# Performance work log

Measured on AMD Instinct MI355X. Metric: run time of the kernel, lower is better.

The kernel has to match this reference:

```python
import jax, jax.numpy as jnp
import numpy as np
import math

# Fixed video latent grid (grid_sizes) and module dims
F_, H_, W_ = 8, 16, 30
FRAME = H_ * W_          # tokens per frame = 480
L = F_ * FRAME           # seq_len = 3840
DIM, NH, HD = 1536, 12, 128
EPS = 1e-6


def _rope_table(maxlen, d):
    # rope_params: angle[t, j] = t / theta^(2j/d), j = 0..d/2-1
    inv = 1.0 / (10000.0 ** (np.arange(0, d, 2, dtype=np.float64) / d))
    return (np.arange(maxlen, dtype=np.float64)[:, None] * inv[None, :]).astype(np.float32)


def _angles(freqs_f, freqs_h, freqs_w):
    # concat per-axis angles -> [F,H,W,HD//2] -> [L, HD//2]
    a = jnp.concatenate([
        jnp.broadcast_to(freqs_f[:F_, None, None, :], (F_, H_, W_, freqs_f.shape[1])),
        jnp.broadcast_to(freqs_h[None, :H_, None, :], (F_, H_, W_, freqs_h.shape[1])),
        jnp.broadcast_to(freqs_w[None, None, :W_, :], (F_, H_, W_, freqs_w.shape[1])),
    ], axis=-1)
    return a.reshape(L, HD // 2)


def _rope(x, ang):
    # x: [B, L, NH, HD]; complex pairs are consecutive along head_dim
    xr, xi = x[..., 0::2], x[..., 1::2]
    c = jnp.cos(ang)[None, :, None, :]
    s = jnp.sin(ang)[None, :, None, :]
    yr = xr * c - xi * s
    yi = xr * s + xi * c
    return jnp.stack([yr, yi], axis=-1).reshape(x.shape)


def _rmsnorm(x, g):
    return x * jax.lax.rsqrt(jnp.mean(x * x, axis=-1, keepdims=True) + EPS) * g


def setup_inputs() -> dict:
    key = jax.random.key(0)
    ks = jax.random.split(key, 6)
    sc = 0.02
    inp = {
        'x': jax.random.normal(ks[0], (1, L, DIM), jnp.float32),
        'Wq': jax.random.normal(ks[1], (DIM, DIM), jnp.float32) * sc,
        'bq': jnp.zeros((DIM,), jnp.float32),
        'Wk': jax.random.normal(ks[2], (DIM, DIM), jnp.float32) * sc,
        'bk': jnp.zeros((DIM,), jnp.float32),
        'Wv': jax.random.normal(ks[3], (DIM, DIM), jnp.float32) * sc,
        'bv': jnp.zeros((DIM,), jnp.float32),
        'Wo': jax.random.normal(ks[4], (DIM, DIM), jnp.float32) * sc,
        'bo': jnp.zeros((DIM,), jnp.float32),
        'gq': jnp.ones((DIM,), jnp.float32),
        'gk': jnp.ones((DIM,), jnp.float32),
        'freqs_f': jnp.asarray(_rope_table(1024, 44)[:F_]),  # 22 complex dims
        'freqs_h': jnp.asarray(_rope_table(1024, 42)[:H_]),  # 21 complex dims
        'freqs_w': jnp.asarray(_rope_table(1024, 42)[:W_]),  # 21 complex dims
    }
    return inp


def reference(x, Wq, bq, Wk, bk, Wv, bv, Wo, bo, gq, gk, freqs_f, freqs_h, freqs_w):
    B = x.shape[0]
    q = _rmsnorm(x @ Wq + bq, gq).reshape(B, L, NH, HD)
    k = _rmsnorm(x @ Wk + bk, gk).reshape(B, L, NH, HD)
    v = (x @ Wv + bv).reshape(B, L, NH, HD)
    ang = _angles(freqs_f, freqs_h, freqs_w)
    q = _rope(q, ang)
    k = _rope(k, ang)
    # frame-level block-causal mask: query frame >= key frame
    frame = jnp.arange(L) // FRAME
    mask = frame[:, None] >= frame[None, :]
    scores = jnp.einsum('bqhd,bkhd->bhqk', q, k) * (1.0 / math.sqrt(HD))
    scores = jnp.where(mask[None, None], scores, -jnp.inf)
    attn = jax.nn.softmax(scores, axis=-1)
    out = jnp.einsum('bhqk,bkhd->bqhd', attn, v).reshape(B, L, DIM)
    return out @ Wo + bo
```

## Files before the change

kernel.cpp:

```cpp
#include <hip/hip_runtime.h>
#include <hip/hip_bf16.h>
#include <math.h>

#define F_    8
#define H_    16
#define W_    30
#define FRAME (H_*W_)
#define L_    (F_*FRAME)
#define DIM   1536
#define NH    12
#define HD    128
#define EPS   1e-6f

#define GM 128
#define GN 128
#define GKT 32

typedef __attribute__((ext_vector_type(8))) short short8;
typedef __attribute__((ext_vector_type(4))) float floatx4;

__device__ __forceinline__ float bf2f(unsigned short u) {
    unsigned int x = ((unsigned int)u) << 16;
    return __uint_as_float(x);
}

__device__ __forceinline__ short f2bs(float f) {
    union { __hip_bfloat16 b; short s; } u;
    u.b = __float2bfloat16(f);
    return u.s;
}

__device__ __forceinline__ bool is_f32_flag(const unsigned int* gq32) {
    return gq32[0] == 0x3F800000u;
}

__device__ __forceinline__ float ldany(const void* p, long i, bool f32) {
    return f32 ? ((const float*)p)[i] : bf2f(((const unsigned short*)p)[i]);
}

__device__ __forceinline__ void gl_lds16(const void* g, void* l) {
    __builtin_amdgcn_global_load_lds(
        (const __attribute__((address_space(1))) unsigned int*)g,
        (__attribute__((address_space(3))) unsigned int*)l,
        16, 0, 0);
}

__global__ __launch_bounds__(256) void k_cossin(const void* Ff, const void* Fh, const void* Fw,
                                                const unsigned int* gq32,
                                                float* cosb, float* sinb) {
    int idx = blockIdx.x * 256 + threadIdx.x;
    if (idx >= L_ * 64) return;
    bool f32 = is_f32_flag(gq32);
    int l = idx >> 6, j = idx & 63;
    int f = l / FRAME;
    int rem = l - f * FRAME;
    int h = rem / W_;
    int w = rem - h * W_;
    float a;
    if (j < 22)      a = ldany(Ff, (long)f * 22 + j, f32);
    else if (j < 43) a = ldany(Fh, (long)h * 21 + (j - 22), f32);
    else             a = ldany(Fw, (long)w * 21 + (j - 43), f32);
    cosb[idx] = cosf(a);
    sinb[idx] = sinf(a);
}

__global__ __launch_bounds__(256) void k_tobf(const void* in, short* out, int n,
                                              const unsigned int* gq32) {
    bool f32 = is_f32_flag(gq32);
    int i = blockIdx.x * 256 + threadIdx.x;
    if (i < n) out[i] = f2bs(ldany(in, i, f32));
}

__global__ __launch_bounds__(256) void k_wt4(const void* W0, const void* W1,
                                             const void* W2, const void* W3,
                                             short* T0, short* T1, short* T2, short* T3,
                                             const unsigned int* gq32) {
    bool f32 = is_f32_flag(gq32);
    int z = blockIdx.z;
    const void* W = z == 0 ? W0 : z == 1 ? W1 : z == 2 ? W2 : W3;
    short* WT     = z == 0 ? T0 : z == 1 ? T1 : z == 2 ? T2 : T3;
    __shared__ float tile[32][33];
    int n0 = blockIdx.x * 32, k0 = blockIdx.y * 32;
    int tx = threadIdx.x & 31, ty = threadIdx.x >> 5;
    for (int i = ty; i < 32; i += 8)
        tile[i][tx] = ldany(W, (long)(k0 + i) * DIM + n0 + tx, f32);
    __syncthreads();
    for (int i = ty; i < 32; i += 8)
        WT[(size_t)(n0 + i) * DIM + k0 + tx] = f2bs(tile[tx][i]);
}

__global__ __launch_bounds__(256) void k_gemm_qkv(const short* A,
                                                  const short* BTq, const short* BTk, const short* BTv,
                                                  const void* bq, const void* bk, const void* bv,
                                                  float* Cq, float* Ck, short* Cv,
                                                  const unsigned int* gq32) {
    bool f32 = is_f32_flag(gq32);
    __shared__ short As[GM * GKT];
    __shared__ short Bs[GN * GKT];

    int sec = blockIdx.x / (DIM / GN);
    int bn  = (blockIdx.x % (DIM / GN)) * GN;
    int bm  = blockIdx.y * GM;
    const short* BT  = sec == 0 ? BTq : sec == 1 ? BTk : BTv;
    const void* bias = sec == 0 ? bq  : sec == 1 ? bk  : bv;

    int tid  = threadIdx.x;
    int wave = tid >> 6, lane = tid & 63;
    int q15 = lane & 15, quad = lane >> 4;
    int wr = wave >> 1, wc = wave & 1;
    int lr = lane >> 2;
    int kc = (lane & 3) * 8;

    floatx4 acc[4][4];
    #pragma unroll
    for (int i = 0; i < 4; ++i)
        #pragma unroll
        for (int j = 0; j < 4; ++j) acc[i][j] = (floatx4)0.f;

    const short* Abase = A  + (size_t)(bm + wave * 32 + lr) * DIM + kc;
    const short* Bbase = BT + (size_t)(bn + wave * 32 + lr) * DIM + kc;
    short* AsW = &As[(wave * 32) * GKT];
    short* BsW = &Bs[(wave * 32) * GKT];

    for (int k0 = 0; k0 < DIM; k0 += GKT) {
        __syncthreads();
        gl_lds16(Abase + k0,                      AsW);
        gl_lds16(Abase + k0 + (size_t)16 * DIM,   AsW + 16 * GKT);
        gl_lds16(Bbase + k0,                      BsW);
        gl_lds16(Bbase + k0 + (size_t)16 * DIM,   BsW + 16 * GKT);
        __syncthreads();

        short8 af[4], bfr[4];
        #pragma unroll
        for (int t = 0; t < 4; ++t) {
            af[t]  = *(const short8*)&As[(wr * 64 + t * 16 + q15) * GKT + quad * 8];
            bfr[t] = *(const short8*)&Bs[(wc * 64 + t * 16 + q15) * GKT + quad * 8];
        }
        #pragma unroll
        for (int i = 0; i < 4; ++i)
            #pragma unroll
            for (int j = 0; j < 4; ++j)
                acc[i][j] = __builtin_amdgcn_mfma_f32_16x16x32_bf16(af[i], bfr[j], acc[i][j], 0, 0, 0);
    }

    #pragma unroll
    for (int i = 0; i < 4; ++i) {
        int row = bm + wr * 64 + i * 16 + quad * 4;
        #pragma unroll
        for (int j = 0; j < 4; ++j) {
            int col = bn + wc * 64 + j * 16 + q15;
            float bv2 = ldany(bias, col, f32);
            #pragma unroll
            for (int r = 0; r < 4; ++r) {
                float v = acc[i][j][r] + bv2;
                size_t oi = (size_t)(row + r) * DIM + col;
                if (sec == 0)      Cq[oi] = v;
                else if (sec == 1) Ck[oi] = v;
                else               Cv[oi] = f2bs(v);
            }
        }
    }
}

__global__ __launch_bounds__(256) void k_gemm_out(const short* A, const short* BT,
                                                  const void* bias, void* Cout,
                                                  const unsigned int* gq32) {
    bool f32 = is_f32_flag(gq32);
    __shared__ short As[GM * GKT];
    __shared__ short Bs[GN * GKT];

    int tid  = threadIdx.x;
    int wave = tid >> 6, lane = tid & 63;
    int q15 = lane & 15, quad = lane >> 4;
    int wr = wave >> 1, wc = wave & 1;
    int lr = lane >> 2;
    int kc = (lane & 3) * 8;

    int bm = blockIdx.y * GM;
    int bn = blockIdx.x * GN;

    floatx4 acc[4][4];
    #pragma unroll
    for (int i = 0; i < 4; ++i)
        #pragma unroll
        for (int j = 0; j < 4; ++j) acc[i][j] = (floatx4)0.f;

    const short* Abase = A  + (size_t)(bm + wave * 32 + lr) * DIM + kc;
    const short* Bbase = BT + (size_t)(bn + wave * 32 + lr) * DIM + kc;
    short* AsW = &As[(wave * 32) * GKT];
    short* BsW = &Bs[(wave * 32) * GKT];

    for (int k0 = 0; k0 < DIM; k0 += GKT) {
        __syncthreads();
        gl_lds16(Abase + k0,                      AsW);
        gl_lds16(Abase + k0 + (size_t)16 * DIM,   AsW + 16 * GKT);
        gl_lds16(Bbase + k0,                      BsW);
        gl_lds16(Bbase + k0 + (size_t)16 * DIM,   BsW + 16 * GKT);
        __syncthreads();

        short8 af[4], bfr[4];
        #pragma unroll
        for (int t = 0; t < 4; ++t) {
            af[t]  = *(const short8*)&As[(wr * 64 + t * 16 + q15) * GKT + quad * 8];
            bfr[t] = *(const short8*)&Bs[(wc * 64 + t * 16 + q15) * GKT + quad * 8];
        }
        #pragma unroll
        for (int i = 0; i < 4; ++i)
            #pragma unroll
            for (int j = 0; j < 4; ++j)
                acc[i][j] = __builtin_amdgcn_mfma_f32_16x16x32_bf16(af[i], bfr[j], acc[i][j], 0, 0, 0);
    }

    #pragma unroll
    for (int i = 0; i < 4; ++i) {
        int row = bm + wr * 64 + i * 16 + quad * 4;
        #pragma unroll
        for (int j = 0; j < 4; ++j) {
            int col = bn + wc * 64 + j * 16 + q15;
            float bv = ldany(bias, col, f32);
            #pragma unroll
            for (int r = 0; r < 4; ++r) {
                float v = acc[i][j][r] + bv;
                size_t oi = (size_t)(row + r) * DIM + col;
                if (f32) ((float*)Cout)[oi] = v;
                else     ((__hip_bfloat16*)Cout)[oi] = __float2bfloat16(v);
            }
        }
    }
}

__global__ __launch_bounds__(256) void k_norm_rope2(const float* qin, const float* kin,
                                                    __hip_bfloat16* qout, __hip_bfloat16* kout,
                                                    const void* gq, const void* gk,
                                                    const float* cosb, const float* sinb,
                                                    const unsigned int* gq32) {
    bool f32 = is_f32_flag(gq32);
    int which = blockIdx.y;
    const float* in = which ? kin : qin;
    __hip_bfloat16* outb = which ? kout : qout;
    const void* g = which ? gk : gq;
    float qk_scale = which ? 1.0f : 0.08838834764831845f;

    int l = blockIdx.x;
    int t = threadIdx.x;
    const float* row = in + (long)l * DIM;
    __hip_bfloat16* orow = outb + (long)l * DIM;

    float ss = 0.f;
    for (int i = t; i < DIM; i += 256) { float xv = row[i]; ss += xv * xv; }
    #pragma unroll
    for (int off = 32; off; off >>= 1) ss += __shfl_xor(ss, off);

    __shared__ float red[4];
    int wid = t >> 6;
    if ((t & 63) == 0) red[wid] = ss;
    __syncthreads();
    float scale = rsqrtf((red[0] + red[1] + red[2] + red[3]) / (float)DIM + EPS) * qk_scale;

    for (int p = t; p < DIM / 2; p += 256) {
        int j = p & 63;
        float c = cosb[l * 64 + j];
        float s = sinb[l * 64 + j];
        float xr = row[2 * p]     * scale * ldany(g, 2 * p,     f32);
        float xi = row[2 * p + 1] * scale * ldany(g, 2 * p + 1, f32);
        orow[2 * p]     = __float2bfloat16(xr * c - xi * s);
        orow[2 * p + 1] = __float2bfloat16(xr * s + xi * c);
    }
}

__global__ __launch_bounds__(256) void k_vt(const short* vbf, short* vtb) {
    __shared__ short tile[32][33];
    int d0 = blockIdx.x * 32;
    int l0 = blockIdx.y * 32;
    int tx = threadIdx.x & 31, ty = threadIdx.x >> 5;
    for (int i = ty; i < 32; i += 8)
        tile[i][tx] = vbf[(size_t)(l0 + i) * DIM + d0 + tx];
    __syncthreads();
    int slot = ((tx & 15) >> 2) * 8 + ((tx >> 4) & 1) * 4 + (tx & 3);
    for (int i = ty; i < 32; i += 8) {
        int d = d0 + i;
        int h = d >> 7, hd = d & 127;
        vtb[((size_t)h * HD + hd) * L_ + l0 + slot] = tile[tx][i];
    }
}

__global__ __launch_bounds__(192, 3) void k_attn7(const short* qbf, const short* kbf,
                                                  const short* vtb,
                                                  float* opart, float* lpart) {
    __shared__ short Ks[2][4][32][32];
    __shared__ short Vs[2][128][32];

    int tid = threadIdx.x;
    int wave = tid >> 6, lane = tid & 63;
    int q15 = lane & 15, quad = lane >> 4;

    int head = blockIdx.x % NH;
    int t = blockIdx.x / NH;
    int rg, kf0, kf1;
    if (t < 30)      { if (t < 25) { rg = 15 + t;        kf0 = 0; kf1 = 3; }
                       else        { rg = 35 + (t - 25); kf0 = 4; kf1 = 7; } }
    else if (t < 40) { int i = t - 30;
                       if (i < 5)  { rg = 10 + i;        kf0 = 0; kf1 = 2; }
                       else        { rg = 30 + (i - 5);  kf0 = 4; kf1 = 6; } }
    else if (t < 50) { int i = t - 40;
                       if (i < 5)  { rg = 5 + i;         kf0 = 0; kf1 = 1; }
                       else        { rg = 25 + (i - 5);  kf0 = 4; kf1 = 5; } }
    else             { int i = t - 50;
                       if (i < 5)  { rg = i;             kf0 = 0; kf1 = 0; }
                       else        { rg = 20 + (i - 5);  kf0 = 4; kf1 = 4; } }

    int qbase  = rg * 96 + wave * 32;
    int kstart = kf0 * FRAME;
    int iters  = (kf1 - kf0 + 1) * (FRAME / 32);
    int slot   = (kf0 == 4) ? 1 : 0;

    const short* kpH = kbf + head * HD;
    const short* vpH = vtb + (size_t)head * HD * L_;

    int sub = lane >> 2;
    int ch  = (lane & 3) * 8;

    for (int i = wave; i < 16; i += 3) {
        if (i < 8) {
            int ks = i >> 1, key = (i & 1) * 16 + sub;
            gl_lds16(kpH + (size_t)(kstart + key) * DIM + ks * 32 + ch,
                     (short*)Ks[0] + i * 512);
        } else {
            int jj = i - 8, d = jj * 16 + sub;
            gl_lds16(vpH + (size_t)d * L_ + kstart + ch,
                     (short*)Vs[0] + jj * 512);
        }
    }

    short8 qf[2][4];
    #pragma unroll
    for (int mi = 0; mi < 2; ++mi)
        #pragma unroll
        for (int ks = 0; ks < 4; ++ks)
            qf[mi][ks] = *(const short8*)(qbf + (size_t)(qbase + mi * 16 + q15) * DIM
                                          + head * HD + ks * 32 + quad * 8);

    floatx4 o[2][8];
    #pragma unroll
    for (int mi = 0; mi < 2; ++mi)
        #pragma unroll
        for (int ct = 0; ct < 8; ++ct) o[mi][ct] = (floatx4)0.f;
    float lp[2] = {0.f, 0.f};

    for (int it = 0; it < iters; ++it) {
        __syncthreads();
        int buf = it & 1;
        if (it + 1 < iters) {
            int kb = kstart + (it + 1) * 32;
            for (int i = wave; i < 16; i += 3) {
                if (i < 8) {
                    int ks = i >> 1, key = (i & 1) * 16 + sub;
                    gl_lds16(kpH + (size_t)(kb + key) * DIM + ks * 32 + ch,
                             (short*)Ks[buf ^ 1] + i * 512);
                } else {
                    int jj = i - 8, d = jj * 16 + sub;
                    gl_lds16(vpH + (size_t)d * L_ + kb + ch,
                             (short*)Vs[buf ^ 1] + jj * 512);
                }
            }
        }

        floatx4 st[2][2];
        #pragma unroll
        for (int nt = 0; nt < 2; ++nt)
            #pragma unroll
            for (int mi = 0; mi < 2; ++mi) st[nt][mi] = (floatx4)0.f;
        #pragma unroll
        for (int ks = 0; ks < 4; ++ks) {
            short8 k0 = *(const short8*)&Ks[buf][ks][q15][quad * 8];
            short8 k1 = *(const short8*)&Ks[buf][ks][16 + q15][quad * 8];
            st[0][0] = __builtin_amdgcn_mfma_f32_16x16x32_bf16(k0, qf[0][ks], st[0][0], 0, 0, 0);
            st[0][1] = __builtin_amdgcn_mfma_f32_16x16x32_bf16(k0, qf[1][ks], st[0][1], 0, 0, 0);
            st[1][0] = __builtin_amdgcn_mfma_f32_16x16x32_bf16(k1, qf[0][ks], st[1][0], 0, 0, 0);
            st[1][1] = __builtin_amdgcn_mfma_f32_16x16x32_bf16(k1, qf[1][ks], st[1][1], 0, 0, 0);
        }

        short8 vf[8];
        #pragma unroll
        for (int ct = 0; ct < 8; ++ct)
            vf[ct] = *(const short8*)&Vs[buf][ct * 16 + q15][quad * 8];

        #pragma unroll
        for (int mi = 0; mi < 2; ++mi) {
            short8 pf;
            float sum = 0.f;
            #pragma unroll
            for (int r = 0; r < 4; ++r) {
                float p0 = __expf(st[0][mi][r]);
                float p1 = __expf(st[1][mi][r]);
                sum += p0 + p1;
                pf[r]     = f2bs(p0);
                pf[4 + r] = f2bs(p1);
            }
            lp[mi] += sum;
            #pragma unroll
            for (int ct = 0; ct < 8; ++ct)
                o[mi][ct] = __builtin_amdgcn_mfma_f32_16x16x32_bf16(vf[ct], pf, o[mi][ct], 0, 0, 0);
        }
    }

    #pragma unroll
    for (int mi = 0; mi < 2; ++mi) {
        float l = lp[mi];
        l += __shfl_xor(l, 16);
        l += __shfl_xor(l, 32);
        int row = qbase + mi * 16 + q15;
        float* orow = opart + (size_t)slot * L_ * DIM + (size_t)row * DIM + head * HD;
        if (quad == 0) lpart[((size_t)slot * L_ + row) * NH + head] = l;
        #pragma unroll
        for (int ct = 0; ct < 8; ++ct)
            *(floatx4*)&orow[ct * 16 + quad * 4] = o[mi][ct];
    }
}

__global__ __launch_bounds__(256) void k_attn_norm2(const float* opart, const float* lpart,
                                                    short* obf) {
    int idx = (blockIdx.x * 256 + threadIdx.x) * 4;
    int row = idx / DIM, col = idx - row * DIM;
    int head = col >> 7;
    float4 v = *(const float4*)(opart + idx);
    float l = lpart[(size_t)row * NH + head];
    if (row >= 4 * FRAME) {
        float4 w = *(const float4*)(opart + (size_t)L_ * DIM + idx);
        v.x += w.x; v.y += w.y; v.z += w.z; v.w += w.w;
        l += lpart[((size_t)L_ + row) * NH + head];
    }
    float inv = 1.f / l;
    short4 s;
    s.x = f2bs(v.x * inv); s.y = f2bs(v.y * inv);
    s.z = f2bs(v.z * inv); s.w = f2bs(v.w * inv);
    *(short4*)(obf + idx) = s;
}

extern "C" void kernel_launch(void* const* d_in, const int* in_sizes, int n_in,
                              void* d_out, int out_size, void* d_ws, size_t ws_size,
                              hipStream_t stream) {
    const void* x  = d_in[0];
    const void* Wq = d_in[1];
    const void* bq = d_in[2];
    const void* Wk = d_in[3];
    const void* bk = d_in[4];
    const void* Wv = d_in[5];
    const void* bv = d_in[6];
    const void* Wo = d_in[7];
    const void* bo = d_in[8];
    const void* gq = d_in[9];
    const void* gk = d_in[10];
    const void* Ff = d_in[11];
    const void* Fh = d_in[12];
    const void* Fw = d_in[13];
    const unsigned int* flagp = (const unsigned int*)gq;

    char* p = (char*)d_ws;
    const size_t LD = (size_t)L_ * DIM;
    const size_t WW = (size_t)DIM * DIM;
    float* cosb = (float*)p;            p += (size_t)L_ * 64 * 4;
    float* sinb = (float*)p;            p += (size_t)L_ * 64 * 4;
    float* qb   = (float*)p;            p += LD * 4;
    float* kb   = (float*)p;            p += LD * 4;
    short* qbf  = (short*)p;            p += LD * 2;
    short* kbf  = (short*)p;            p += LD * 2;
    short* vtb  = (short*)p;            p += LD * 2;
    short* vbf  = (short*)p;            p += LD * 2;
    short* xb   = (short*)p;            p += LD * 2;
    short* WqT  = (short*)p;            p += WW * 2;
    short* WkT  = (short*)p;            p += WW * 2;
    short* WvT  = (short*)p;            p += WW * 2;
    short* WoT  = (short*)p;            p += WW * 2;
    float* opart = (float*)p;           p += 2 * LD * 4;
    float* lpart = (float*)p;           p += (size_t)2 * L_ * NH * 4;
    short* obf  = (short*)qb;

    hipLaunchKernelGGL(k_cossin, dim3((L_ * 64) / 256), dim3(256), 0, stream,
                       Ff, Fh, Fw, flagp, cosb, sinb);
    hipLaunchKernelGGL(k_tobf, dim3((int)(LD / 256)), dim3(256), 0, stream,
                       x, xb, (int)LD, flagp);
    hipLaunchKernelGGL(k_wt4, dim3(DIM / 32, DIM / 32, 4), dim3(256), 0, stream,
                       Wq, Wk, Wv, Wo, WqT, WkT, WvT, WoT, flagp);

    hipLaunchKernelGGL(k_gemm_qkv, dim3(3 * (DIM / GN), L_ / GM), dim3(256), 0, stream,
                       xb, WqT, WkT, WvT, bq, bk, bv, qb, kb, vbf, flagp);

    hipLaunchKernelGGL(k_norm_rope2, dim3(L_, 2), dim3(256), 0, stream,
                       qb, kb, (__hip_bfloat16*)qbf, (__hip_bfloat16*)kbf,
                       gq, gk, cosb, sinb, flagp);
    hipLaunchKernelGGL(k_vt, dim3(DIM / 32, L_ / 32), dim3(256), 0, stream, vbf, vtb);

    hipLaunchKernelGGL(k_attn7, dim3(60 * NH), dim3(192), 0, stream,
                       qbf, kbf, vtb, opart, lpart);
    hipLaunchKernelGGL(k_attn_norm2, dim3((int)(LD / 1024)), dim3(256), 0, stream,
                       opart, lpart, obf);

    hipLaunchKernelGGL(k_gemm_out, dim3(DIM / GN, L_ / GM), dim3(256), 0, stream,
                       obf, WoT, bo, d_out, flagp);
}
```

Baseline: 397.4 us.

## Split attention into fixed 2-frame key chunks with XOR-swizzled LDS and XCD-aware block mapping

Attention work is split into uniform chunks of two key frames (30 iterations, or 15 for the diagonal half-chunk), so the grid grows from 720 to 1200 blocks of near-equal length and loads balance across CUs. Up to four partial outputs are written and the normalization kernel sums a variable number of them per row. K/V tiles share one LDS buffer with an XOR swizzle to cut bank conflicts, and global source pointers are precomputed and advanced each stage. Blocks are remapped so consecutive heads land on the same XCD, and occupancy is raised to 4 blocks per CU. In exchange, partial-result memory traffic grows and the reduction kernel reads more data.

```diff
diff --git a/kernel.cpp b/kernel.cpp
--- a/kernel.cpp
+++ b/kernel.cpp
@@ -284,53 +284,75 @@
     }
 }
 
-__global__ __launch_bounds__(192, 3) void k_attn7(const short* qbf, const short* kbf,
+#define STAGE(b) do {                                              \
+    _Pragma("unroll")                                              \
+    for (int n_ = 0; n_ < 6; ++n_) {                               \
+        int i_ = wave + 3 * n_;                                    \
+        if (i_ < 16) {                                             \
+            gl_lds16(gsrc[n_], &SB[b][i_ * 512]);                  \
+            gsrc[n_] += (i_ < 8) ? 32 * DIM : 32;                  \
+        }                                                          \
+    }                                                              \
+} while (0)
+
+__global__ __launch_bounds__(192, 4) void k_attn8(const short* qbf, const short* kbf,
                                                   const short* vtb,
                                                   float* opart, float* lpart) {
-    __shared__ short Ks[2][4][32][32];
-    __shared__ short Vs[2][128][32];
+    __shared__ short SB[2][8192];
 
     int tid = threadIdx.x;
     int wave = tid >> 6, lane = tid & 63;
     int q15 = lane & 15, quad = lane >> 4;
 
-    int head = blockIdx.x % NH;
-    int t = blockIdx.x / NH;
-    int rg, kf0, kf1;
-    if (t < 30)      { if (t < 25) { rg = 15 + t;        kf0 = 0; kf1 = 3; }
-                       else        { rg = 35 + (t - 25); kf0 = 4; kf1 = 7; } }
-    else if (t < 40) { int i = t - 30;
-                       if (i < 5)  { rg = 10 + i;        kf0 = 0; kf1 = 2; }
-                       else        { rg = 30 + (i - 5);  kf0 = 4; kf1 = 6; } }
-    else if (t < 50) { int i = t - 40;
-                       if (i < 5)  { rg = 5 + i;         kf0 = 0; kf1 = 1; }
-                       else        { rg = 25 + (i - 5);  kf0 = 4; kf1 = 5; } }
-    else             { int i = t - 50;
-                       if (i < 5)  { rg = i;             kf0 = 0; kf1 = 0; }
-                       else        { rg = 20 + (i - 5);  kf0 = 4; kf1 = 4; } }
+    int v = (blockIdx.x % 8) * 150 + blockIdx.x / 8;
+    int head = v / 100;
+    int t = v % 100;
+    int rg, c, iters;
+    if (t < 80) {
+        int fq, base, hc;
+        if (t < 5)       { fq = 1; base = 0;  hc = 1; }
+        else if (t < 10) { fq = 2; base = 5;  hc = 1; }
+        else if (t < 20) { fq = 3; base = 10; hc = 2; }
+        else if (t < 30) { fq = 4; base = 20; hc = 2; }
+        else if (t < 45) { fq = 5; base = 30; hc = 3; }
+        else if (t < 60) { fq = 6; base = 45; hc = 3; }
+        else             { fq = 7; base = 60; hc = 4; }
+        int idx = t - base;
+        rg = fq * 5 + idx / hc;
+        c  = idx % hc;
+        iters = 30;
+    } else {
+        int idx = t - 80;
+        int fq = (idx / 5) * 2;
+        rg = fq * 5 + idx % 5;
+        c  = fq >> 1;
+        iters = 15;
+    }
 
     int qbase  = rg * 96 + wave * 32;
-    int kstart = kf0 * FRAME;
-    int iters  = (kf1 - kf0 + 1) * (FRAME / 32);
-    int slot   = (kf0 == 4) ? 1 : 0;
+    int kstart = c * 960;
 
     const short* kpH = kbf + head * HD;
     const short* vpH = vtb + (size_t)head * HD * L_;
 
     int sub = lane >> 2;
-    int ch  = (lane & 3) * 8;
-
-    for (int i = wave; i < 16; i += 3) {
-        if (i < 8) {
-            int ks = i >> 1, key = (i & 1) * 16 + sub;
-            gl_lds16(kpH + (size_t)(kstart + key) * DIM + ks * 32 + ch,
-                     (short*)Ks[0] + i * 512);
+    int chs = ((lane & 3) ^ ((sub >> 1) & 3)) * 8;
+
+    const short* gsrc[6];
+    #pragma unroll
+    for (int n = 0; n < 6; ++n) {
+        int i = wave + 3 * n;
+        int ii = (i < 16) ? i : 0;
+        if (ii < 8) {
+            int ks = ii >> 1, key = (ii & 1) * 16 + sub;
+            gsrc[n] = kpH + (size_t)(kstart + key) * DIM + ks * 32 + chs;
         } else {
-            int jj = i - 8, d = jj * 16 + sub;
-            gl_lds16(vpH + (size_t)d * L_ + kstart + ch,
-                     (short*)Vs[0] + jj * 512);
-        }
-    }
+            int jj = ii - 8, d = jj * 16 + sub;
+            gsrc[n] = vpH + (size_t)d * L_ + kstart + chs;
+        }
+    }
+
+    STAGE(0);
 
     short8 qf[2][4];
     #pragma unroll
@@ -347,23 +369,15 @@
         for (int ct = 0; ct < 8; ++ct) o[mi][ct] = (floatx4)0.f;
     float lp[2] = {0.f, 0.f};
 
+    int sw = (quad ^ ((q15 >> 1) & 3)) * 8;
+
     for (int it = 0; it < iters; ++it) {
         __syncthreads();
         int buf = it & 1;
-        if (it + 1 < iters) {
-            int kb = kstart + (it + 1) * 32;
-            for (int i = wave; i < 16; i += 3) {
-                if (i < 8) {
-                    int ks = i >> 1, key = (i & 1) * 16 + sub;
-                    gl_lds16(kpH + (size_t)(kb + key) * DIM + ks * 32 + ch,
-                             (short*)Ks[buf ^ 1] + i * 512);
-                } else {
-                    int jj = i - 8, d = jj * 16 + sub;
-                    gl_lds16(vpH + (size_t)d * L_ + kb + ch,
-                             (short*)Vs[buf ^ 1] + jj * 512);
-                }
-            }
-        }
+        if (it + 1 < iters) STAGE(buf ^ 1);
+
+        const short* Kb = &SB[buf][0];
+        const short* Vb = &SB[buf][4096];
 
         floatx4 st[2][2];
         #pragma unroll
@@ -372,8 +386,8 @@
             for (int mi = 0; mi < 2; ++mi) st[nt][mi] = (floatx4)0.f;
         #pragma unroll
         for (int ks = 0; ks < 4; ++ks) {
-            short8 k0 = *(const short8*)&Ks[buf][ks][q15][quad * 8];
-            short8 k1 = *(const short8*)&Ks[buf][ks][16 + q15][quad * 8];
+            short8 k0 = *(const short8*)&Kb[ks * 1024 + q15 * 32 + sw];
+            short8 k1 = *(const short8*)&Kb[ks * 1024 + 512 + q15 * 32 + sw];
             st[0][0] = __builtin_amdgcn_mfma_f32_16x16x32_bf16(k0, qf[0][ks], st[0][0], 0, 0, 0);
             st[0][1] = __builtin_amdgcn_mfma_f32_16x16x32_bf16(k0, qf[1][ks], st[0][1], 0, 0, 0);
             st[1][0] = __builtin_amdgcn_mfma_f32_16x16x32_bf16(k1, qf[0][ks], st[1][0], 0, 0, 0);
@@ -383,7 +397,7 @@
         short8 vf[8];
         #pragma unroll
         for (int ct = 0; ct < 8; ++ct)
-            vf[ct] = *(const short8*)&Vs[buf][ct * 16 + q15][quad * 8];
+            vf[ct] = *(const short8*)&Vb[(ct * 16 + q15) * 32 + sw];
 
         #pragma unroll
         for (int mi = 0; mi < 2; ++mi) {
@@ -410,31 +424,32 @@
         l += __shfl_xor(l, 16);
         l += __shfl_xor(l, 32);
         int row = qbase + mi * 16 + q15;
-        float* orow = opart + (size_t)slot * L_ * DIM + (size_t)row * DIM + head * HD;
-        if (quad == 0) lpart[((size_t)slot * L_ + row) * NH + head] = l;
+        float* orow = opart + (size_t)c * L_ * DIM + (size_t)row * DIM + head * HD;
+        if (quad == 0) lpart[((size_t)c * L_ + row) * NH + head] = l;
         #pragma unroll
         for (int ct = 0; ct < 8; ++ct)
             *(floatx4*)&orow[ct * 16 + quad * 4] = o[mi][ct];
     }
 }
 
-__global__ __launch_bounds__(256) void k_attn_norm2(const float* opart, const float* lpart,
+__global__ __launch_bounds__(256) void k_attn_norm4(const float* opart, const float* lpart,
                                                     short* obf) {
     int idx = (blockIdx.x * 256 + threadIdx.x) * 4;
     int row = idx / DIM, col = idx - row * DIM;
     int head = col >> 7;
-    float4 v = *(const float4*)(opart + idx);
+    int ns = (row / FRAME) / 2 + 1;
+    float4 vv = *(const float4*)(opart + idx);
     float l = lpart[(size_t)row * NH + head];
-    if (row >= 4 * FRAME) {
-        float4 w = *(const float4*)(opart + (size_t)L_ * DIM + idx);
-        v.x += w.x; v.y += w.y; v.z += w.z; v.w += w.w;
-        l += lpart[((size_t)L_ + row) * NH + head];
+    for (int s = 1; s < ns; ++s) {
+        float4 w = *(const float4*)(opart + (size_t)s * L_ * DIM + idx);
+        vv.x += w.x; vv.y += w.y; vv.z += w.z; vv.w += w.w;
+        l += lpart[((size_t)s * L_ + row) * NH + head];
     }
     float inv = 1.f / l;
-    short4 s;
-    s.x = f2bs(v.x * inv); s.y = f2bs(v.y * inv);
-    s.z = f2bs(v.z * inv); s.w = f2bs(v.w * inv);
-    *(short4*)(obf + idx) = s;
+    short4 s4;
+    s4.x = f2bs(vv.x * inv); s4.y = f2bs(vv.y * inv);
+    s4.z = f2bs(vv.z * inv); s4.w = f2bs(vv.w * inv);
+    *(short4*)(obf + idx) = s4;
 }
 
 extern "C" void kernel_launch(void* const* d_in, const int* in_sizes, int n_in,
@@ -472,8 +487,8 @@
     short* WkT  = (short*)p;            p += WW * 2;
     short* WvT  = (short*)p;            p += WW * 2;
     short* WoT  = (short*)p;            p += WW * 2;
-    float* opart = (float*)p;           p += 2 * LD * 4;
-    float* lpart = (float*)p;           p += (size_t)2 * L_ * NH * 4;
+    float* opart = (float*)p;           p += 4 * LD * 4;
+    float* lpart = (float*)p;           p += (size_t)4 * L_ * NH * 4;
     short* obf  = (short*)qb;
 
     hipLaunchKernelGGL(k_cossin, dim3((L_ * 64) / 256), dim3(256), 0, stream,
@@ -491,9 +506,9 @@
                        gq, gk, cosb, sinb, flagp);
     hipLaunchKernelGGL(k_vt, dim3(DIM / 32, L_ / 32), dim3(256), 0, stream, vbf, vtb);
 
-    hipLaunchKernelGGL(k_attn7, dim3(60 * NH), dim3(192), 0, stream,
+    hipLaunchKernelGGL(k_attn8, dim3(100 * NH), dim3(192), 0, stream,
                        qbf, kbf, vtb, opart, lpart);
-    hipLaunchKernelGGL(k_attn_norm2, dim3((int)(LD / 1024)), dim3(256), 0, stream,
+    hipLaunchKernelGGL(k_attn_norm4, dim3((int)(LD / 1024)), dim3(256), 0, stream,
                        opart, lpart, obf);
 
     hipLaunchKernelGGL(k_gemm_out, dim3(DIM / GN, L_ / GM), dim3(256), 0, stream,
```

After: 677.4 us. +70.5%, slower.

## Repartition causal attention into 3-way key splits with 6-wave blocks sharing K/V tiles

Applied to the files above, without the earlier changes.

Replaces the hard-coded 2-way key-frame split with a table-driven schedule that splits keys into chunks of up to three frames (three partial slots). Each block now runs six waves covering two query row-groups, so one K/V tile load in shared memory serves twice as many queries. The goal is to cut redundant K/V traffic and balance work across blocks. The cost is a three-slot partial buffer and a combine pass that reads up to three partials per row. Some waves duplicate work when a block has only one row group.

```diff
diff --git a/kernel.cpp b/kernel.cpp
--- a/kernel.cpp
+++ b/kernel.cpp
@@ -284,9 +284,25 @@
     }
 }
 
-__global__ __launch_bounds__(192, 3) void k_attn7(const short* qbf, const short* kbf,
-                                                  const short* vtb,
-                                                  float* opart, float* lpart) {
+#define TT(a,b,k,n,s) ((unsigned)((a)|((b)<<6)|((k)<<12)|((n)<<15)|((s)<<17)))
+static __device__ const unsigned int TTAB[41] = {
+    TT(10,11,0,3,0), TT(12,13,0,3,0), TT(14,15,0,3,0), TT(16,17,0,3,0),
+    TT(18,19,0,3,0), TT(20,21,0,3,0), TT(22,23,0,3,0), TT(24,25,0,3,0),
+    TT(26,27,0,3,0), TT(28,29,0,3,0), TT(30,31,0,3,0), TT(32,33,0,3,0),
+    TT(34,35,0,3,0), TT(36,37,0,3,0), TT(38,39,0,3,0),
+    TT(25,26,3,3,1), TT(27,28,3,3,1), TT(29,30,3,3,1), TT(31,32,3,3,1),
+    TT(33,34,3,3,1), TT(35,36,3,3,1), TT(37,38,3,3,1), TT(39,39,3,3,1),
+    TT(35,36,6,2,2), TT(37,38,6,2,2), TT(39,39,6,2,2),
+    TT(20,21,3,2,1), TT(22,23,3,2,1), TT(24,24,3,2,1),
+    TT(5,6,0,2,0),   TT(7,8,0,2,0),   TT(9,9,0,2,0),
+    TT(30,31,6,1,2), TT(32,33,6,1,2), TT(34,34,6,1,2),
+    TT(15,16,3,1,1), TT(17,18,3,1,1), TT(19,19,3,1,1),
+    TT(0,1,0,1,0),   TT(2,3,0,1,0),   TT(4,4,0,1,0)
+};
+
+__global__ __launch_bounds__(384, 3) void k_attn10(const short* qbf, const short* kbf,
+                                                   const short* vtb,
+                                                   float* opart, float* lpart) {
     __shared__ short Ks[2][4][32][32];
     __shared__ short Vs[2][128][32];
 
@@ -296,23 +312,16 @@
 
     int head = blockIdx.x % NH;
     int t = blockIdx.x / NH;
-    int rg, kf0, kf1;
-    if (t < 30)      { if (t < 25) { rg = 15 + t;        kf0 = 0; kf1 = 3; }
-                       else        { rg = 35 + (t - 25); kf0 = 4; kf1 = 7; } }
-    else if (t < 40) { int i = t - 30;
-                       if (i < 5)  { rg = 10 + i;        kf0 = 0; kf1 = 2; }
-                       else        { rg = 30 + (i - 5);  kf0 = 4; kf1 = 6; } }
-    else if (t < 50) { int i = t - 40;
-                       if (i < 5)  { rg = 5 + i;         kf0 = 0; kf1 = 1; }
-                       else        { rg = 25 + (i - 5);  kf0 = 4; kf1 = 5; } }
-    else             { int i = t - 50;
-                       if (i < 5)  { rg = i;             kf0 = 0; kf1 = 0; }
-                       else        { rg = 20 + (i - 5);  kf0 = 4; kf1 = 4; } }
-
-    int qbase  = rg * 96 + wave * 32;
+    unsigned e = TTAB[t];
+    int rgA = e & 63, rgB = (e >> 6) & 63;
+    int kf0 = (e >> 12) & 7, nf = (e >> 15) & 3, c = (e >> 17) & 3;
+    int iters  = nf * 15;
     int kstart = kf0 * FRAME;
-    int iters  = (kf1 - kf0 + 1) * (FRAME / 32);
-    int slot   = (kf0 == 4) ? 1 : 0;
+
+    int w3 = wave < 3 ? wave : wave - 3;
+    int rg = wave < 3 ? rgA : rgB;
+    int qbase = rg * 96 + w3 * 32;
+    bool dup = (rgA == rgB) && (wave >= 3);
 
     const short* kpH = kbf + head * HD;
     const short* vpH = vtb + (size_t)head * HD * L_;
@@ -320,7 +329,7 @@
     int sub = lane >> 2;
     int ch  = (lane & 3) * 8;
 
-    for (int i = wave; i < 16; i += 3) {
+    for (int i = wave; i < 16; i += 6) {
         if (i < 8) {
             int ks = i >> 1, key = (i & 1) * 16 + sub;
             gl_lds16(kpH + (size_t)(kstart + key) * DIM + ks * 32 + ch,
@@ -352,7 +361,7 @@
         int buf = it & 1;
         if (it + 1 < iters) {
             int kb = kstart + (it + 1) * 32;
-            for (int i = wave; i < 16; i += 3) {
+            for (int i = wave; i < 16; i += 6) {
                 if (i < 8) {
                     int ks = i >> 1, key = (i & 1) * 16 + sub;
                     gl_lds16(kpH + (size_t)(kb + key) * DIM + ks * 32 + ch,
@@ -404,37 +413,40 @@
         }
     }
 
-    #pragma unroll
-    for (int mi = 0; mi < 2; ++mi) {
-        float l = lp[mi];
-        l += __shfl_xor(l, 16);
-        l += __shfl_xor(l, 32);
-        int row = qbase + mi * 16 + q15;
-        float* orow = opart + (size_t)slot * L_ * DIM + (size_t)row * DIM + head * HD;
-        if (quad == 0) lpart[((size_t)slot * L_ + row) * NH + head] = l;
-        #pragma unroll
-        for (int ct = 0; ct < 8; ++ct)
-            *(floatx4*)&orow[ct * 16 + quad * 4] = o[mi][ct];
-    }
-}
-
-__global__ __launch_bounds__(256) void k_attn_norm2(const float* opart, const float* lpart,
+    if (!dup) {
+        #pragma unroll
+        for (int mi = 0; mi < 2; ++mi) {
+            float l = lp[mi];
+            l += __shfl_xor(l, 16);
+            l += __shfl_xor(l, 32);
+            int row = qbase + mi * 16 + q15;
+            float* orow = opart + (size_t)c * L_ * DIM + (size_t)row * DIM + head * HD;
+            if (quad == 0) lpart[((size_t)c * L_ + row) * NH + head] = l;
+            #pragma unroll
+            for (int ct = 0; ct < 8; ++ct)
+                *(floatx4*)&orow[ct * 16 + quad * 4] = o[mi][ct];
+        }
+    }
+}
+
+__global__ __launch_bounds__(256) void k_attn_norm6(const float* opart, const float* lpart,
                                                     short* obf) {
     int idx = (blockIdx.x * 256 + threadIdx.x) * 4;
     int row = idx / DIM, col = idx - row * DIM;
     int head = col >> 7;
-    float4 v = *(const float4*)(opart + idx);
+    int ns = row / (3 * FRAME) + 1;
+    float4 vv = *(const float4*)(opart + idx);
     float l = lpart[(size_t)row * NH + head];
-    if (row >= 4 * FRAME) {
-        float4 w = *(const float4*)(opart + (size_t)L_ * DIM + idx);
-        v.x += w.x; v.y += w.y; v.z += w.z; v.w += w.w;
-        l += lpart[((size_t)L_ + row) * NH + head];
+    for (int s = 1; s < ns; ++s) {
+        float4 w = *(const float4*)(opart + (size_t)s * L_ * DIM + idx);
+        vv.x += w.x; vv.y += w.y; vv.z += w.z; vv.w += w.w;
+        l += lpart[((size_t)s * L_ + row) * NH + head];
     }
     float inv = 1.f / l;
-    short4 s;
-    s.x = f2bs(v.x * inv); s.y = f2bs(v.y * inv);
-    s.z = f2bs(v.z * inv); s.w = f2bs(v.w * inv);
-    *(short4*)(obf + idx) = s;
+    short4 s4;
+    s4.x = f2bs(vv.x * inv); s4.y = f2bs(vv.y * inv);
+    s4.z = f2bs(vv.z * inv); s4.w = f2bs(vv.w * inv);
+    *(short4*)(obf + idx) = s4;
 }
 
 extern "C" void kernel_launch(void* const* d_in, const int* in_sizes, int n_in,
@@ -472,8 +484,8 @@
     short* WkT  = (short*)p;            p += WW * 2;
     short* WvT  = (short*)p;            p += WW * 2;
     short* WoT  = (short*)p;            p += WW * 2;
-    float* opart = (float*)p;           p += 2 * LD * 4;
-    float* lpart = (float*)p;           p += (size_t)2 * L_ * NH * 4;
+    float* opart = (float*)p;           p += 3 * LD * 4;
+    float* lpart = (float*)p;           p += (size_t)3 * L_ * NH * 4;
     short* obf  = (short*)qb;
 
     hipLaunchKernelGGL(k_cossin, dim3((L_ * 64) / 256), dim3(256), 0, stream,
@@ -491,9 +503,9 @@
                        gq, gk, cosb, sinb, flagp);
     hipLaunchKernelGGL(k_vt, dim3(DIM / 32, L_ / 32), dim3(256), 0, stream, vbf, vtb);
 
-    hipLaunchKernelGGL(k_attn7, dim3(60 * NH), dim3(192), 0, stream,
+    hipLaunchKernelGGL(k_attn10, dim3(41 * NH), dim3(384), 0, stream,
                        qbf, kbf, vtb, opart, lpart);
-    hipLaunchKernelGGL(k_attn_norm2, dim3((int)(LD / 1024)), dim3(256), 0, stream,
+    hipLaunchKernelGGL(k_attn_norm6, dim3((int)(LD / 1024)), dim3(256), 0, stream,
                        opart, lpart, obf);
 
     hipLaunchKernelGGL(k_gemm_out, dim3(DIM / GN, L_ / GM), dim3(256), 0, stream,
```

After: 420.1 us. 1.06x slower.

## Triple-buffer K/V tiles in attention with prefetch depth two and explicit vmcnt waits

Applied to the files above, without the earlier changes.

Moves the attention kernel from double to triple buffering of the K and V LDS tiles. Loads are now issued two iterations ahead and waited on with per-wave s_waitcnt vmcnt counts plus a raw s_barrier, in place of a full __syncthreads each iteration. The goal is to hide global-to-LDS latency behind more MFMA work. The cost is 50% more LDS per block, which could lower occupancy. Correctness now depends on hand-tuned vmcnt values that must match the number of loads each wave issues.

```diff
diff --git a/kernel.cpp b/kernel.cpp
--- a/kernel.cpp
+++ b/kernel.cpp
@@ -284,11 +284,25 @@
     }
 }
 
-__global__ __launch_bounds__(192, 3) void k_attn7(const short* qbf, const short* kbf,
-                                                  const short* vtb,
-                                                  float* opart, float* lpart) {
-    __shared__ short Ks[2][4][32][32];
-    __shared__ short Vs[2][128][32];
+#define STAGE3(kb, b) do {                                              \
+    for (int i_ = wave; i_ < 16; i_ += 3) {                             \
+        if (i_ < 8) {                                                   \
+            int ks_ = i_ >> 1, key_ = (i_ & 1) * 16 + sub;              \
+            gl_lds16(kpH + (size_t)((kb) + key_) * DIM + ks_ * 32 + ch, \
+                     (short*)Ks[b] + i_ * 512);                         \
+        } else {                                                        \
+            int jj_ = i_ - 8, d_ = jj_ * 16 + sub;                      \
+            gl_lds16(vpH + (size_t)d_ * L_ + (kb) + ch,                 \
+                     (short*)Vs[b] + jj_ * 512);                        \
+        }                                                               \
+    }                                                                   \
+} while (0)
+
+__global__ __launch_bounds__(192, 3) void k_attn11(const short* qbf, const short* kbf,
+                                                   const short* vtb,
+                                                   float* opart, float* lpart) {
+    __shared__ short Ks[3][4][32][32];
+    __shared__ short Vs[3][128][32];
 
     int tid = threadIdx.x;
     int wave = tid >> 6, lane = tid & 63;
@@ -320,17 +334,8 @@
     int sub = lane >> 2;
     int ch  = (lane & 3) * 8;
 
-    for (int i = wave; i < 16; i += 3) {
-        if (i < 8) {
-            int ks = i >> 1, key = (i & 1) * 16 + sub;
-            gl_lds16(kpH + (size_t)(kstart + key) * DIM + ks * 32 + ch,
-                     (short*)Ks[0] + i * 512);
-        } else {
-            int jj = i - 8, d = jj * 16 + sub;
-            gl_lds16(vpH + (size_t)d * L_ + kstart + ch,
-                     (short*)Vs[0] + jj * 512);
-        }
-    }
+    STAGE3(kstart, 0);
+    STAGE3(kstart + 32, 1);
 
     short8 qf[2][4];
     #pragma unroll
@@ -340,6 +345,9 @@
             qf[mi][ks] = *(const short8*)(qbf + (size_t)(qbase + mi * 16 + q15) * DIM
                                           + head * HD + ks * 32 + quad * 8);
 
+    asm volatile("s_waitcnt vmcnt(0)" ::: "memory");
+    __builtin_amdgcn_sched_barrier(0);
+
     floatx4 o[2][8];
     #pragma unroll
     for (int mi = 0; mi < 2; ++mi)
@@ -347,22 +355,17 @@
         for (int ct = 0; ct < 8; ++ct) o[mi][ct] = (floatx4)0.f;
     float lp[2] = {0.f, 0.f};
 
+    int bcur = 0;
     for (int it = 0; it < iters; ++it) {
-        __syncthreads();
-        int buf = it & 1;
-        if (it + 1 < iters) {
-            int kb = kstart + (it + 1) * 32;
-            for (int i = wave; i < 16; i += 3) {
-                if (i < 8) {
-                    int ks = i >> 1, key = (i & 1) * 16 + sub;
-                    gl_lds16(kpH + (size_t)(kb + key) * DIM + ks * 32 + ch,
-                             (short*)Ks[buf ^ 1] + i * 512);
-                } else {
-                    int jj = i - 8, d = jj * 16 + sub;
-                    gl_lds16(vpH + (size_t)d * L_ + kb + ch,
-                             (short*)Vs[buf ^ 1] + jj * 512);
-                }
-            }
+        if (it >= 2) {
+            if (wave == 0) asm volatile("s_waitcnt vmcnt(6)" ::: "memory");
+            else           asm volatile("s_waitcnt vmcnt(5)" ::: "memory");
+        }
+        __builtin_amdgcn_s_barrier();
+        __builtin_amdgcn_sched_barrier(0);
+        if (it + 2 < iters) {
+            int bpre = bcur >= 1 ? bcur - 1 : 2;
+            STAGE3(kstart + (it + 2) * 32, bpre);
         }
 
         floatx4 st[2][2];
@@ -372,8 +375,8 @@
             for (int mi = 0; mi < 2; ++mi) st[nt][mi] = (floatx4)0.f;
         #pragma unroll
         for (int ks = 0; ks < 4; ++ks) {
-            short8 k0 = *(const short8*)&Ks[buf][ks][q15][quad * 8];
-            short8 k1 = *(const short8*)&Ks[buf][ks][16 + q15][quad * 8];
+            short8 k0 = *(const short8*)&Ks[bcur][ks][q15][quad * 8];
+            short8 k1 = *(const short8*)&Ks[bcur][ks][16 + q15][quad * 8];
             st[0][0] = __builtin_amdgcn_mfma_f32_16x16x32_bf16(k0, qf[0][ks], st[0][0], 0, 0, 0);
             st[0][1] = __builtin_amdgcn_mfma_f32_16x16x32_bf16(k0, qf[1][ks], st[0][1], 0, 0, 0);
             st[1][0] = __builtin_amdgcn_mfma_f32_16x16x32_bf16(k1, qf[0][ks], st[1][0], 0, 0, 0);
@@ -383,7 +386,7 @@
         short8 vf[8];
         #pragma unroll
         for (int ct = 0; ct < 8; ++ct)
-            vf[ct] = *(const short8*)&Vs[buf][ct * 16 + q15][quad * 8];
+            vf[ct] = *(const short8*)&Vs[bcur][ct * 16 + q15][quad * 8];
 
         #pragma unroll
         for (int mi = 0; mi < 2; ++mi) {
@@ -402,6 +405,8 @@
             for (int ct = 0; ct < 8; ++ct)
                 o[mi][ct] = __builtin_amdgcn_mfma_f32_16x16x32_bf16(vf[ct], pf, o[mi][ct], 0, 0, 0);
         }
+
+        bcur = bcur < 2 ? bcur + 1 : 0;
     }
 
     #pragma unroll
@@ -491,7 +496,7 @@
                        gq, gk, cosb, sinb, flagp);
     hipLaunchKernelGGL(k_vt, dim3(DIM / 32, L_ / 32), dim3(256), 0, stream, vbf, vtb);
 
-    hipLaunchKernelGGL(k_attn7, dim3(60 * NH), dim3(192), 0, stream,
+    hipLaunchKernelGGL(k_attn11, dim3(60 * NH), dim3(192), 0, stream,
                        qbf, kbf, vtb, opart, lpart);
     hipLaunchKernelGGL(k_attn_norm2, dim3((int)(LD / 1024)), dim3(256), 0, stream,
                        opart, lpart, obf);
```

New measurement: 404.2 us. No clear change (+1.7%).
